# Kernel tuning notes

Hardware: AMD Instinct MI355X
Metric: run time of the kernel (lower is better)

The kernel has to match this reference:

```python
import jax, jax.numpy as jnp
import numpy as np

B, S, H, T, DI, HID, K, HEADS = 8, 1024, 768, 8, 64, 128, 8, 2
NEG = 1.0e12


def _build_adj(spans):
    # spans: [K,3] int; returns [K+1,K+1] edge multiplicity matrix (dst, src)
    s, e = spans[:, 0], spans[:, 1]
    same = (s[:, None] == s[None, :]) & (e[:, None] == e[None, :])
    # contain[i,j]: span i strictly contains span j (source appends this edge twice)
    contain = (s[:, None] <= s[None, :]) & (e[None, :] <= e[:, None]) & (~same)
    N = K + 1
    adj = jnp.eye(N, dtype=jnp.float32)                    # PyG add_self_loops
    adj = adj.at[1:, 0].add(1.0)                           # global -> span i
    adj = adj.at[0, 1:].add(1.0)                           # span i -> global
    adj = adj.at[1:, 1:].add(2.0 * contain.T.astype(jnp.float32))
    return adj


def _gat(x, adj, W, a_src, a_dst, b):
    # x [N,F]; adj [N,N] multiplicity with layout (dst, src). PyG GATConv math.
    N = x.shape[0]
    h = (x @ W).reshape(N, HEADS, -1)                      # [N,Hd,D]
    asrc = jnp.einsum('nhd,hd->nh', h, a_src)
    adst = jnp.einsum('nhd,hd->nh', h, a_dst)
    ee = jax.nn.leaky_relu(adst[:, None, :] + asrc[None, :, :], 0.2)  # [dst,src,Hd]
    logmult = jnp.where(adj > 0, jnp.log(jnp.maximum(adj, 1e-20)), 0.0)
    scores = jnp.where(adj[:, :, None] > 0, ee + logmult[:, :, None], -1e30)
    attn = jax.nn.softmax(scores, axis=1)                  # softmax over source nodes
    out = jnp.einsum('dsh,shf->dhf', attn, h).reshape(N, -1)
    return out + b


def _layernorm(x, g, bta):
    mu = x.mean(-1, keepdims=True)
    var = x.var(-1, keepdims=True)
    return (x - mu) / jnp.sqrt(var + 1e-5) * g + bta


def _forward(hidden, attention_mask, spans, W1, a_src1, a_dst1, b1, ln_g, ln_b,
             W2, a_src2, a_dst2, b2, dense_W, dense_b,
             g_centers, g_sigmas, g_weights, corr):
    start, end, etype = spans[..., 0], spans[..., 1], spans[..., 2]  # [B,K]
    pos = jnp.arange(S)
    span_mask = ((pos[None, None, :] >= start[..., None]) &
                 (pos[None, None, :] <= end[..., None])).astype(hidden.dtype)  # [B,K,S]
    span_len = (end - start + 1).astype(hidden.dtype)
    span_feat = jnp.einsum('bks,bsh->bkh', span_mask, hidden) / span_len[..., None]
    global_feat = hidden.mean(axis=1, keepdims=True)                 # [B,1,H]
    nodes = jnp.concatenate([global_feat, span_feat], axis=1)        # [B,K+1,H]
    adj = jax.vmap(_build_adj)(spans)                                # [B,K+1,K+1]

    g1 = jax.vmap(lambda x, a: _gat(x, a, W1, a_src1, a_dst1, b1))(nodes, adj)
    g1 = _layernorm(jax.nn.relu(g1), ln_g, ln_b)
    g2 = jax.vmap(lambda x, a: _gat(x, a, W2, a_src2, a_dst2, b2))(g1, adj)
    g2 = jax.nn.relu(g2)
    enhanced = g2.mean(axis=1)                                       # per-graph mean pool [B,2*HID]

    cover = span_mask.sum(axis=1)                                    # [B,S] how many spans cover token s
    token_enh = cover[..., None] * enhanced[:, None, :]              # [B,S,2*HID]
    combined = jnp.concatenate([hidden, token_enh], axis=-1)

    qk = (combined @ dense_W + dense_b).reshape(B, S, T, 2 * DI)
    qw, kw = qk[..., :DI], qk[..., DI:]

    # RoPE (sin/cos interleaved exactly as in source)
    inv = jnp.power(10000.0, -2.0 * jnp.arange(DI // 2) / DI)
    ang = pos[:, None].astype(jnp.float32) * inv[None, :]            # [S,DI/2]
    sin = jnp.repeat(jnp.sin(ang), 2, axis=-1)[None, :, None, :]     # [1,S,1,DI]
    cos = jnp.repeat(jnp.cos(ang), 2, axis=-1)[None, :, None, :]

    def rot(v):
        v2 = jnp.stack([-v[..., 1::2], v[..., ::2]], axis=-1).reshape(v.shape)
        return v * cos + v2 * sin

    qw, kw = rot(qw), rot(kw)

    logits = jnp.einsum('bmtd,bntd->btmn', qw, kw)                   # [B,T,S,S]

    # multi-modal gaussian kernel span maps (vectorized over batch/span/component)
    pf = pos.astype(jnp.float32)
    dxs = pf[None, None, None, :] - start[..., None, None] - g_centers[None, None, :, None]
    dxe = pf[None, None, None, :] - end[..., None, None] - g_centers[None, None, :, None]
    Ksr = g_weights[None, None, :, None] * jnp.exp(-0.5 * (dxs / g_sigmas[None, None, :, None]) ** 2)
    Ken = g_weights[None, None, :, None] * jnp.exp(-0.5 * (dxe / g_sigmas[None, None, :, None]) ** 2)
    gmap = jnp.einsum('bkcm,bkcn->bkmn', Ksr, Ken)                   # [B,K,S,S]
    corr_span = corr[etype]                                          # [B,K,T]
    logits = logits + jnp.einsum('bkt,bkmn->btmn', corr_span, gmap)

    pad = attention_mask[:, None, None, :]                           # key-dim-only mask (as in source)
    logits = logits * pad - (1.0 - pad) * NEG
    tril = jnp.tril(jnp.ones((S, S), logits.dtype), -1)
    logits = logits - tril * NEG
    return logits / jnp.sqrt(jnp.float32(DI))


def setup_inputs() -> dict:
    key = jax.random.key(0)
    ks = jax.random.split(key, 16)
    hidden = jax.random.normal(ks[0], (B, S, H), jnp.float32)
    attention_mask = jnp.ones((B, S), jnp.float32)
    start = jax.random.randint(ks[1], (B, K), 0, S - 32)
    length = jax.random.randint(ks[2], (B, K), 1, 16)
    spans = jnp.stack([start, start + length,
                       jax.random.randint(ks[3], (B, K), 0, T)], axis=-1).astype(jnp.int32)
    sd = 0.05
    return {
        'hidden': hidden,
        'attention_mask': attention_mask,
        'spans': spans,
        'W1': jax.random.normal(ks[4], (H, HEADS * HID), jnp.float32) * sd,
        'a_src1': jax.random.normal(ks[5], (HEADS, HID), jnp.float32) * sd,
        'a_dst1': jax.random.normal(ks[6], (HEADS, HID), jnp.float32) * sd,
        'b1': jnp.zeros((HEADS * HID,), jnp.float32),
        'ln_g': jnp.ones((HEADS * HID,), jnp.float32),
        'ln_b': jnp.zeros((HEADS * HID,), jnp.float32),
        'W2': jax.random.normal(ks[7], (HEADS * HID, HEADS * HID), jnp.float32) * sd,
        'a_src2': jax.random.normal(ks[8], (HEADS, HID), jnp.float32) * sd,
        'a_dst2': jax.random.normal(ks[9], (HEADS, HID), jnp.float32) * sd,
        'b2': jnp.zeros((HEADS * HID,), jnp.float32),
        'dense_W': jax.random.normal(ks[10], (H + HEADS * HID, T * 2 * DI), jnp.float32) * sd,
        'dense_b': jnp.zeros((T * 2 * DI,), jnp.float32),
        'g_centers': jnp.array([0.0, 0.0], jnp.float32),
        'g_sigmas': jnp.array([1.0, 3.0], jnp.float32),
        'g_weights': jnp.array([0.5, 0.5], jnp.float32),
        'corr': jnp.eye(T, dtype=jnp.float32),
    }


def reference(hidden, attention_mask, spans, W1, a_src1, a_dst1, b1, ln_g, ln_b,
              W2, a_src2, a_dst2, b2, dense_W, dense_b,
              g_centers, g_sigmas, g_weights, corr):
    return _forward(hidden, attention_mask, spans, W1, a_src1, a_dst1, b1, ln_g, ln_b,
                    W2, a_src2, a_dst2, b2, dense_W, dense_b,
                    g_centers, g_sigmas, g_weights, corr)
```

## Files before the change

kernel.cpp:

```cpp
#include <hip/hip_runtime.h>
#include <cstdint>
#include <cstddef>

#define BB 8
#define SS 1024
#define HH 768
#define TT 8
#define DII 64
#define HIDD 128
#define KSP 8
#define NHEADS 2
#define NNODES 9
#define GDIM 256
#define CDIM 1024
#define DAUGP 96
#define NEGV 1e12f

using bf16x8 = __attribute__((ext_vector_type(8))) __bf16;
using f32x4  = __attribute__((ext_vector_type(4))) float;

static __device__ inline unsigned short f2bf(float x) {
  union { float f; unsigned u; } v; v.f = x;
  unsigned r = v.u + 0x7fff + ((v.u >> 16) & 1);
  return (unsigned short)(r >> 16);
}

__global__ void kc1b_cvt_partial(const float* __restrict__ hidden,
                                 unsigned short* __restrict__ hbf,
                                 float* __restrict__ part) {
  int z = blockIdx.x, b = blockIdx.y, tid = threadIdx.x;
  const float* hb = hidden + (size_t)b * SS * HH;
  unsigned short* ho = hbf + (size_t)b * SS * HH;
  #pragma unroll
  for (int j = 0; j < 3; j++) {
    int c = tid + j * 256;
    float acc = 0.f;
    #pragma unroll 8
    for (int r = z * 64; r < z * 64 + 64; r++) {
      float v = hb[(size_t)r * HH + c];
      ho[(size_t)r * HH + c] = f2bf(v);
      acc += v;
    }
    part[((size_t)b * 16 + z) * HH + c] = acc;
  }
}

__global__ void kc2_cvt_wtop(const float* __restrict__ dense_W, unsigned short* __restrict__ WtopT) {
  __shared__ float t[32][33];
  int k0 = blockIdx.x * 32, n0 = blockIdx.y * 32;
  int tid = threadIdx.x;
  int r = tid >> 3, c4 = (tid & 7) * 4;
  float4 v = *(const float4*)&dense_W[(size_t)(k0 + r) * CDIM + n0 + c4];
  t[r][c4 + 0] = v.x; t[r][c4 + 1] = v.y; t[r][c4 + 2] = v.z; t[r][c4 + 3] = v.w;
  __syncthreads();
  int ro = tid >> 3, co4 = (tid & 7) * 4;
  ushort4 o;
  o.x = f2bf(t[co4 + 0][ro]); o.y = f2bf(t[co4 + 1][ro]);
  o.z = f2bf(t[co4 + 2][ro]); o.w = f2bf(t[co4 + 3][ro]);
  *(ushort4*)&WtopT[(size_t)(n0 + ro) * HH + k0 + co4] = o;
}

__global__ void k1a_spans(const float* __restrict__ hidden, const int* __restrict__ spans,
                          float* __restrict__ nodes, float* __restrict__ cover) {
  int k = blockIdx.x, b = blockIdx.y, tid = threadIdx.x;
  __shared__ int sp[KSP * 3];
  if (tid < KSP * 3) sp[tid] = spans[b * KSP * 3 + tid];
  __syncthreads();
  if (tid < 128) {
    int s = k * 128 + tid;
    float c = 0.f;
    #pragma unroll
    for (int kk = 0; kk < KSP; kk++)
      c += (s >= sp[kk * 3] && s <= sp[kk * 3 + 1]) ? 1.f : 0.f;
    cover[b * SS + s] = c;
  }
  int st = sp[k * 3], en = sp[k * 3 + 1];
  float inv = 1.f / (float)(en - st + 1);
  const float* hb = hidden + (size_t)b * SS * HH;
  #pragma unroll
  for (int ci = 0; ci < 3; ci++) {
    int c = tid + ci * 256;
    float a = 0.f;
    #pragma unroll
    for (int j = 0; j < 16; j++) {
      int s = st + j;
      int sc = (s <= en) ? s : en;
      float v = hb[(size_t)sc * HH + c];
      a += (s <= en) ? v : 0.f;
    }
    nodes[((size_t)b * NNODES + (k + 1)) * HH + c] = a * inv;
  }
}

__global__ __launch_bounds__(512) void k2_gat(
    const float* __restrict__ part, const float* __restrict__ nodes_g,
    const int* __restrict__ spans,
    const float* __restrict__ W1, const float* __restrict__ a_src1,
    const float* __restrict__ a_dst1, const float* __restrict__ b1,
    const float* __restrict__ ln_g, const float* __restrict__ ln_b,
    const float* __restrict__ W2, const float* __restrict__ a_src2,
    const float* __restrict__ a_dst2, const float* __restrict__ b2,
    float* __restrict__ enhg) {
  int b = blockIdx.x, tid = threadIdx.x;
  __shared__ __align__(16) float nod[NNODES * HH];
  __shared__ __align__(16) float hbuf[NNODES * GDIM];
  __shared__ __align__(16) float gbuf[NNODES * GDIM];
  __shared__ __align__(16) float pbuf[2 * NNODES * GDIM];
  __shared__ float asrc[NNODES * NHEADS], adst[NNODES * NHEADS];
  __shared__ float adjm[NNODES * NNODES];
  __shared__ float attn[NNODES * NNODES * NHEADS];
  __shared__ float mu_s[NNODES], rs_s[NNODES];
  __shared__ int sp[KSP * 3];
  if (tid < KSP * 3) sp[tid] = spans[b * KSP * 3 + tid];
  for (int c = tid; c < HH; c += 512) {
    float s = 0.f;
    #pragma unroll
    for (int z = 0; z < 16; z++) s += part[((size_t)b * 16 + z) * HH + c];
    nod[c] = s * (1.f / (float)SS);
  }
  for (int i = tid; i < (NNODES - 1) * HH; i += 512)
    nod[HH + i] = nodes_g[(size_t)b * NNODES * HH + HH + i];
  __syncthreads();
  {
    int col = tid & 255, h = tid >> 8;
    float acc[NNODES];
    #pragma unroll
    for (int n = 0; n < NNODES; n++) acc[n] = 0.f;
    int dlo = h * 384;
    #pragma unroll 2
    for (int d0 = dlo; d0 < dlo + 384; d0 += 4) {
      float4 nv[NNODES];
      #pragma unroll
      for (int n = 0; n < NNODES; n++) nv[n] = *(const float4*)&nod[n * HH + d0];
      float w0 = W1[(size_t)(d0 + 0) * GDIM + col];
      float w1 = W1[(size_t)(d0 + 1) * GDIM + col];
      float w2 = W1[(size_t)(d0 + 2) * GDIM + col];
      float w3 = W1[(size_t)(d0 + 3) * GDIM + col];
      #pragma unroll
      for (int n = 0; n < NNODES; n++)
        acc[n] += nv[n].x * w0 + nv[n].y * w1 + nv[n].z * w2 + nv[n].w * w3;
    }
    #pragma unroll
    for (int n = 0; n < NNODES; n++) pbuf[(h * NNODES + n) * GDIM + col] = acc[n];
  }
  __syncthreads();
  if (tid < GDIM) {
    #pragma unroll
    for (int n = 0; n < NNODES; n++)
      hbuf[n * GDIM + tid] = pbuf[n * GDIM + tid] + pbuf[(NNODES + n) * GDIM + tid];
  } else if (tid < 256 + NNODES * NNODES) {
    int q = tid - 256;
    int i = q / NNODES, j = q % NNODES;
    float a = (i == j) ? 1.f : 0.f;
    if (i > 0 && j == 0) a += 1.f;
    if (i == 0 && j > 0) a += 1.f;
    if (i > 0 && j > 0 && i != j) {
      int x = j - 1, y = i - 1;
      int sx = sp[x * 3], ex = sp[x * 3 + 1], sy = sp[y * 3], ey = sp[y * 3 + 1];
      bool same = (sx == sy) && (ex == ey);
      if (sx <= sy && ey <= ex && !same) a += 2.f;
    }
    adjm[q] = a;
  }
  __syncthreads();
  if (tid < NNODES * NHEADS) {
    int n = tid >> 1, hd = tid & 1;
    float sa = 0.f, sd = 0.f;
    #pragma unroll 8
    for (int f = 0; f < HIDD; f++) {
      float v = hbuf[n * GDIM + hd * HIDD + f];
      sa += v * a_src1[hd * HIDD + f];
      sd += v * a_dst1[hd * HIDD + f];
    }
    asrc[tid] = sa; adst[tid] = sd;
  }
  __syncthreads();
  if (tid < NNODES * NHEADS) {
    int d = tid >> 1, hd = tid & 1;
    float sc[NNODES]; float mx = -1e30f;
    for (int s2 = 0; s2 < NNODES; s2++) {
      float a = adjm[d * NNODES + s2]; float v;
      if (a > 0.f) {
        float e = adst[d * 2 + hd] + asrc[s2 * 2 + hd];
        e = (e > 0.f) ? e : 0.2f * e;
        v = e + __logf(a);
      } else v = -1e30f;
      sc[s2] = v; mx = fmaxf(mx, v);
    }
    float ssum = 0.f;
    for (int s2 = 0; s2 < NNODES; s2++) { float ex = __expf(sc[s2] - mx); sc[s2] = ex; ssum += ex; }
    float inv = 1.f / ssum;
    for (int s2 = 0; s2 < NNODES; s2++) attn[(d * NNODES + s2) * NHEADS + hd] = sc[s2] * inv;
  }
  __syncthreads();
  if (tid < 256) {
    int hd = tid >> 7;
    float bbv = b1[tid];
    for (int d = 0; d < NNODES; d++) {
      float acc = bbv;
      #pragma unroll
      for (int s2 = 0; s2 < NNODES; s2++)
        acc += attn[(d * NNODES + s2) * NHEADS + hd] * hbuf[s2 * GDIM + tid];
      gbuf[d * GDIM + tid] = fmaxf(acc, 0.f);
    }
  }
  __syncthreads();
  if (tid < NNODES) {
    float s1 = 0.f, s2v = 0.f;
    #pragma unroll 8
    for (int o = 0; o < GDIM; o++) { float v = gbuf[tid * GDIM + o]; s1 += v; s2v += v * v; }
    float mu = s1 / (float)GDIM;
    float var = s2v / (float)GDIM - mu * mu;
    mu_s[tid] = mu; rs_s[tid] = rsqrtf(var + 1e-5f);
  }
  __syncthreads();
  if (tid < 256) {
    float g = ln_g[tid], bt = ln_b[tid];
    for (int d = 0; d < NNODES; d++)
      gbuf[d * GDIM + tid] = (gbuf[d * GDIM + tid] - mu_s[d]) * rs_s[d] * g + bt;
  }
  __syncthreads();
  {
    int col = tid & 255, h = tid >> 8;
    float acc[NNODES];
    #pragma unroll
    for (int n = 0; n < NNODES; n++) acc[n] = 0.f;
    int dlo = h * 128;
    #pragma unroll 2
    for (int d0 = dlo; d0 < dlo + 128; d0 += 4) {
      float4 nv[NNODES];
      #pragma unroll
      for (int n = 0; n < NNODES; n++) nv[n] = *(const float4*)&gbuf[n * GDIM + d0];
      float w0 = W2[(size_t)(d0 + 0) * GDIM + col];
      float w1 = W2[(size_t)(d0 + 1) * GDIM + col];
      float w2 = W2[(size_t)(d0 + 2) * GDIM + col];
      float w3 = W2[(size_t)(d0 + 3) * GDIM + col];
      #pragma unroll
      for (int n = 0; n < NNODES; n++)
        acc[n] += nv[n].x * w0 + nv[n].y * w1 + nv[n].z * w2 + nv[n].w * w3;
    }
    #pragma unroll
    for (int n = 0; n < NNODES; n++) pbuf[(h * NNODES + n) * GDIM + col] = acc[n];
  }
  __syncthreads();
  if (tid < GDIM) {
    #pragma unroll
    for (int n = 0; n < NNODES; n++)
      hbuf[n * GDIM + tid] = pbuf[n * GDIM + tid] + pbuf[(NNODES + n) * GDIM + tid];
  }
  __syncthreads();
  if (tid < NNODES * NHEADS) {
    int n = tid >> 1, hd = tid & 1;
    float sa = 0.f, sd = 0.f;
    #pragma unroll 8
    for (int f = 0; f < HIDD; f++) {
      float v = hbuf[n * GDIM + hd * HIDD + f];
      sa += v * a_src2[hd * HIDD + f];
      sd += v * a_dst2[hd * HIDD + f];
    }
    asrc[tid] = sa; adst[tid] = sd;
  }
  __syncthreads();
  if (tid < NNODES * NHEADS) {
    int d = tid >> 1, hd = tid & 1;
    float sc[NNODES]; float mx = -1e30f;
    for (int s2 = 0; s2 < NNODES; s2++) {
      float a = adjm[d * NNODES + s2]; float v;
      if (a > 0.f) {
        float e = adst[d * 2 + hd] + asrc[s2 * 2 + hd];
        e = (e > 0.f) ? e : 0.2f * e;
        v = e + __logf(a);
      } else v = -1e30f;
      sc[s2] = v; mx = fmaxf(mx, v);
    }
    float ssum = 0.f;
    for (int s2 = 0; s2 < NNODES; s2++) { float ex = __expf(sc[s2] - mx); sc[s2] = ex; ssum += ex; }
    float inv = 1.f / ssum;
    for (int s2 = 0; s2 < NNODES; s2++) attn[(d * NNODES + s2) * NHEADS + hd] = sc[s2] * inv;
  }
  __syncthreads();
  if (tid < 256) {
    int hd = tid >> 7;
    float bbv = b2[tid];
    float msum = 0.f;
    for (int d = 0; d < NNODES; d++) {
      float acc = bbv;
      #pragma unroll
      for (int s2 = 0; s2 < NNODES; s2++)
        acc += attn[(d * NNODES + s2) * NHEADS + hd] * hbuf[s2 * GDIM + tid];
      msum += fmaxf(acc, 0.f);
    }
    enhg[b * GDIM + tid] = msum / 9.f;
  }
}

__global__ void k2b_e2(const float* __restrict__ enhg, const float* __restrict__ dense_W,
                       float* __restrict__ E2) {
  int b = blockIdx.y, tid = threadIdx.x;
  int o = blockIdx.x * 256 + tid;
  __shared__ __align__(16) float eh[GDIM];
  eh[tid] = enhg[b * GDIM + tid];
  __syncthreads();
  float acc = 0.f;
  #pragma unroll 2
  for (int d = 0; d < GDIM; d += 4) {
    float4 ev = *(const float4*)&eh[d];
    acc += ev.x * dense_W[(size_t)(HH + d + 0) * CDIM + o];
    acc += ev.y * dense_W[(size_t)(HH + d + 1) * CDIM + o];
    acc += ev.z * dense_W[(size_t)(HH + d + 2) * CDIM + o];
    acc += ev.w * dense_W[(size_t)(HH + d + 3) * CDIM + o];
  }
  E2[b * CDIM + o] = acc;
}

__global__ __launch_bounds__(256) void k3_dense(
    const unsigned short* __restrict__ hbf, const unsigned short* __restrict__ WtopT,
    const float* __restrict__ dense_b, const float* __restrict__ cover,
    const float* __restrict__ E2,
    unsigned short* __restrict__ Qa, unsigned short* __restrict__ Ka) {
  __shared__ unsigned short As[128 * 40];
  __shared__ unsigned short Bs[128 * 40];
  int tid = threadIdx.x;
  int n0 = blockIdx.x * 128, m0 = blockIdx.y * 128;
  int wave = tid >> 6, lane = tid & 63;
  int wr = wave >> 1, wc = wave & 1;
  int colL = lane & 15, quad = lane >> 4;
  f32x4 acc[4][4];
  #pragma unroll
  for (int i = 0; i < 4; i++)
    #pragma unroll
    for (int j = 0; j < 4; j++) { acc[i][j][0] = 0.f; acc[i][j][1] = 0.f; acc[i][j][2] = 0.f; acc[i][j][3] = 0.f; }
  for (int k0 = 0; k0 < HH; k0 += 32) {
    uint4 va[2], vb[2];
    #pragma unroll
    for (int it = 0; it < 2; it++) {
      int idx = tid + it * 256;
      int r = idx >> 2, seg = idx & 3;
      va[it] = *(const uint4*)(hbf + (size_t)(m0 + r) * HH + k0 + seg * 8);
      vb[it] = *(const uint4*)(WtopT + (size_t)(n0 + r) * HH + k0 + seg * 8);
    }
    __syncthreads();
    #pragma unroll
    for (int it = 0; it < 2; it++) {
      int idx = tid + it * 256;
      int r = idx >> 2, seg = idx & 3;
      *(uint4*)&As[r * 40 + seg * 8] = va[it];
      *(uint4*)&Bs[r * 40 + seg * 8] = vb[it];
    }
    __syncthreads();
    bf16x8 af[4], bf[4];
    #pragma unroll
    for (int tm = 0; tm < 4; tm++)
      af[tm] = *(const bf16x8*)&As[(wr * 64 + tm * 16 + colL) * 40 + quad * 8];
    #pragma unroll
    for (int tn = 0; tn < 4; tn++)
      bf[tn] = *(const bf16x8*)&Bs[(wc * 64 + tn * 16 + colL) * 40 + quad * 8];
    #pragma unroll
    for (int tm = 0; tm < 4; tm++)
      #pragma unroll
      for (int tn = 0; tn < 4; tn++)
        acc[tm][tn] = __builtin_amdgcn_mfma_f32_16x16x32_bf16(af[tm], bf[tn], acc[tm][tn], 0, 0, 0);
  }
  int b = m0 >> 10;
  const float LOG1E4_32 = 0.28782313662425576f;
  unsigned short* __restrict__ dst = (wc == 0) ? Qa : Ka;
  #pragma unroll
  for (int tn = 0; tn < 4; tn++) {
    int col = n0 + wc * 64 + tn * 16 + colL;
    float e2 = E2[b * CDIM + col];
    float db = dense_b[col];
    int t = col >> 7;
    int dd = tn * 16 + colL;
    int i0 = dd >> 1;
    float inv = __expf(-(float)i0 * LOG1E4_32);
    float sgn = (dd & 1) ? 1.f : -1.f;
    size_t tbase = (size_t)(b * TT + t) * SS;
    #pragma unroll
    for (int tm = 0; tm < 4; tm++) {
      int rbase = m0 + wr * 64 + tm * 16 + quad * 4;
      #pragma unroll
      for (int r = 0; r < 4; r++) {
        int m = rbase + r;
        int s = m & 1023;
        float w = acc[tm][tn][r] + cover[m] * e2 + db;
        float p = __shfl_xor(w, 1, 64);
        float sn, cs;
        __sincosf((float)s * inv, &sn, &cs);
        float o = w * cs + sgn * p * sn;
        dst[(tbase + s) * DAUGP + dd] = f2bf(o);
      }
    }
  }
}

__global__ void k4g_gauss(const int* __restrict__ spans, const float* __restrict__ corr,
                          const float* __restrict__ gc, const float* __restrict__ gs,
                          const float* __restrict__ gw,
                          unsigned short* __restrict__ Qa, unsigned short* __restrict__ Ka) {
  int tid = threadIdx.x;
  int g = tid >> 5, lane = tid & 31;
  int row = blockIdx.x * 8 + g;
  int b = row >> 10, s = row & 1023;
  int j = lane & 15;
  int kp = j >> 1, c = j & 1;
  int st = spans[(b * KSP + kp) * 3 + 0];
  int en = spans[(b * KSP + kp) * 3 + 1];
  int et = spans[(b * KSP + kp) * 3 + 2];
  float sig = gs[c], wgt = gw[c], ce = gc[c];
  if (lane < 16) {
    float dx = ((float)(s - st) - ce) / sig;
    float e = wgt * __expf(-0.5f * dx * dx);
    #pragma unroll
    for (int t = 0; t < TT; t++) {
      size_t base = ((size_t)(b * TT + t) * SS + s) * DAUGP;
      Qa[base + 64 + j] = f2bf(corr[et * TT + t] * e);
      Qa[base + 80 + j] = 0;
    }
  } else {
    float dx = ((float)(s - en) - ce) / sig;
    unsigned short bv = f2bf(wgt * __expf(-0.5f * dx * dx));
    #pragma unroll
    for (int t = 0; t < TT; t++) {
      size_t base = ((size_t)(b * TT + t) * SS + s) * DAUGP;
      Ka[base + 64 + j] = bv;
      Ka[base + 80 + j] = 0;
    }
  }
}

__global__ __launch_bounds__(256) void k5_logits(
    const unsigned short* __restrict__ Qa, const unsigned short* __restrict__ Ka,
    const float* __restrict__ amask, float* __restrict__ out) {
  int bz = blockIdx.z; int b = bz >> 3;
  int n0 = blockIdx.x * 128, m0 = blockIdx.y * 128;
  int tid = threadIdx.x;
  if (n0 + 127 < m0) {
    int r0 = tid >> 5, c4 = (tid & 31) * 4;
    float4 pv = *(const float4*)&amask[b * SS + n0 + c4];
    float4 o;
    o.x = (-(1.f - pv.x) * NEGV - NEGV) * 0.125f;
    o.y = (-(1.f - pv.y) * NEGV - NEGV) * 0.125f;
    o.z = (-(1.f - pv.z) * NEGV - NEGV) * 0.125f;
    o.w = (-(1.f - pv.w) * NEGV - NEGV) * 0.125f;
    for (int r = r0; r < 128; r += 8)
      *(float4*)&out[((size_t)bz * SS + m0 + r) * SS + n0 + c4] = o;
    return;
  }
  __shared__ unsigned short Qs[128 * 104];
  __shared__ unsigned short Ks[128 * 104];
  const unsigned short* Qrow = Qa + ((size_t)bz * SS + m0) * DAUGP;
  const unsigned short* Krow = Ka + ((size_t)bz * SS + n0) * DAUGP;
  #pragma unroll
  for (int it = 0; it < 6; it++) {
    int idx = tid + it * 256;
    int r = idx / 12, seg = idx % 12;
    uint4 vq = *(const uint4*)(Qrow + (size_t)r * DAUGP + seg * 8);
    uint4 vk = *(const uint4*)(Krow + (size_t)r * DAUGP + seg * 8);
    *(uint4*)&Qs[r * 104 + seg * 8] = vq;
    *(uint4*)&Ks[r * 104 + seg * 8] = vk;
  }
  __syncthreads();
  int wave = tid >> 6, lane = tid & 63;
  int wr = wave >> 1, wc = wave & 1;
  int colL = lane & 15, quad = lane >> 4;
  f32x4 acc[4][4];
  #pragma unroll
  for (int i = 0; i < 4; i++)
    #pragma unroll
    for (int j = 0; j < 4; j++) { acc[i][j][0] = 0.f; acc[i][j][1] = 0.f; acc[i][j][2] = 0.f; acc[i][j][3] = 0.f; }
  #pragma unroll
  for (int ks = 0; ks < 3; ks++) {
    bf16x8 af[4], bf[4];
    #pragma unroll
    for (int tm = 0; tm < 4; tm++)
      af[tm] = *(const bf16x8*)&Qs[(wr * 64 + tm * 16 + colL) * 104 + ks * 32 + quad * 8];
    #pragma unroll
    for (int tn = 0; tn < 4; tn++)
      bf[tn] = *(const bf16x8*)&Ks[(wc * 64 + tn * 16 + colL) * 104 + ks * 32 + quad * 8];
    #pragma unroll
    for (int tm = 0; tm < 4; tm++)
      #pragma unroll
      for (int tn = 0; tn < 4; tn++)
        acc[tm][tn] = __builtin_amdgcn_mfma_f32_16x16x32_bf16(af[tm], bf[tn], acc[tm][tn], 0, 0, 0);
  }
  #pragma unroll
  for (int tn = 0; tn < 4; tn++) {
    int col = n0 + wc * 64 + tn * 16 + colL;
    float p = amask[b * SS + col];
    float negp = -(1.f - p) * NEGV;
    #pragma unroll
    for (int tm = 0; tm < 4; tm++) {
      int rbase = m0 + wr * 64 + tm * 16 + quad * 4;
      #pragma unroll
      for (int r = 0; r < 4; r++) {
        int m = rbase + r;
        float v = acc[tm][tn][r] * p + negp;
        if (col < m) v -= NEGV;
        out[((size_t)bz * SS + m) * SS + col] = v * 0.125f;
      }
    }
  }
}

extern "C" void kernel_launch(void* const* d_in, const int* in_sizes, int n_in,
                              void* d_out, int out_size, void* d_ws, size_t ws_size,
                              hipStream_t stream) {
  const float* hidden  = (const float*)d_in[0];
  const float* amask   = (const float*)d_in[1];
  const int*   spans   = (const int*)d_in[2];
  const float* W1      = (const float*)d_in[3];
  const float* a_src1  = (const float*)d_in[4];
  const float* a_dst1  = (const float*)d_in[5];
  const float* b1      = (const float*)d_in[6];
  const float* ln_g    = (const float*)d_in[7];
  const float* ln_b    = (const float*)d_in[8];
  const float* W2      = (const float*)d_in[9];
  const float* a_src2  = (const float*)d_in[10];
  const float* a_dst2  = (const float*)d_in[11];
  const float* b2      = (const float*)d_in[12];
  const float* dense_W = (const float*)d_in[13];
  const float* dense_b = (const float*)d_in[14];
  const float* gc      = (const float*)d_in[15];
  const float* gs      = (const float*)d_in[16];
  const float* gw      = (const float*)d_in[17];
  const float* corr    = (const float*)d_in[18];

  char* wsb = (char*)d_ws;
  unsigned short* hbf  = (unsigned short*)wsb;                wsb += (size_t)BB * SS * HH * 2;
  unsigned short* WtopT= (unsigned short*)wsb;                wsb += (size_t)CDIM * HH * 2;
  unsigned short* Qa   = (unsigned short*)wsb;                wsb += (size_t)BB * TT * SS * DAUGP * 2;
  unsigned short* Ka   = (unsigned short*)wsb;                wsb += (size_t)BB * TT * SS * DAUGP * 2;
  float* nodes         = (float*)wsb;                         wsb += (size_t)BB * NNODES * HH * 4;
  float* cover         = (float*)wsb;                         wsb += (size_t)BB * SS * 4;
  float* E2            = (float*)wsb;                         wsb += (size_t)BB * CDIM * 4;
  float* enhg          = (float*)wsb;                         wsb += (size_t)BB * GDIM * 4;
  float* part          = (float*)wsb;                         wsb += (size_t)BB * 16 * HH * 4;
  float* outp = (float*)d_out;

  kc1b_cvt_partial<<<dim3(16, BB), 256, 0, stream>>>(hidden, hbf, part);
  kc2_cvt_wtop<<<dim3(HH / 32, CDIM / 32), 256, 0, stream>>>(dense_W, WtopT);
  k1a_spans<<<dim3(KSP, BB), 256, 0, stream>>>(hidden, spans, nodes, cover);
  k4g_gauss<<<(BB * SS) / 8, 256, 0, stream>>>(spans, corr, gc, gs, gw, Qa, Ka);
  k2_gat<<<BB, 512, 0, stream>>>(part, nodes, spans, W1, a_src1, a_dst1, b1, ln_g, ln_b,
                                 W2, a_src2, a_dst2, b2, enhg);
  k2b_e2<<<dim3(CDIM / 256, BB), 256, 0, stream>>>(enhg, dense_W, E2);
  k3_dense<<<dim3(CDIM / 128, (BB * SS) / 128), 256, 0, stream>>>(hbf, WtopT, dense_b,
                                                                  cover, E2, Qa, Ka);
  k5_logits<<<dim3(8, 8, BB * TT), 256, 0, stream>>>(Qa, Ka, amask, outp);
}
```

Before: 559.9 us.

## Merge prep kernels into one launch and fold E2 projection into GAT kernel

Four independent preprocessing kernels (bf16 conversion with partial sums, weight transpose, span pooling, gaussian feature fill) are merged into one kernel that dispatches on block index. The E2 projection is moved into the tail of the GAT kernel, so the enhg round trip and a separate launch go away. The GAT matmul loops also get a larger unroll. This cuts launch overhead and lets small workloads run side by side, but the E2 product now runs on only 8 blocks, which may serialize that step.

```diff
diff --git a/kernel.cpp b/kernel.cpp
--- a/kernel.cpp
+++ b/kernel.cpp
@@ -25,70 +25,110 @@
   return (unsigned short)(r >> 16);
 }
 
-__global__ void kc1b_cvt_partial(const float* __restrict__ hidden,
-                                 unsigned short* __restrict__ hbf,
-                                 float* __restrict__ part) {
-  int z = blockIdx.x, b = blockIdx.y, tid = threadIdx.x;
-  const float* hb = hidden + (size_t)b * SS * HH;
-  unsigned short* ho = hbf + (size_t)b * SS * HH;
-  #pragma unroll
-  for (int j = 0; j < 3; j++) {
-    int c = tid + j * 256;
-    float acc = 0.f;
-    #pragma unroll 8
-    for (int r = z * 64; r < z * 64 + 64; r++) {
-      float v = hb[(size_t)r * HH + c];
-      ho[(size_t)r * HH + c] = f2bf(v);
-      acc += v;
-    }
-    part[((size_t)b * 16 + z) * HH + c] = acc;
-  }
-}
-
-__global__ void kc2_cvt_wtop(const float* __restrict__ dense_W, unsigned short* __restrict__ WtopT) {
-  __shared__ float t[32][33];
-  int k0 = blockIdx.x * 32, n0 = blockIdx.y * 32;
-  int tid = threadIdx.x;
-  int r = tid >> 3, c4 = (tid & 7) * 4;
-  float4 v = *(const float4*)&dense_W[(size_t)(k0 + r) * CDIM + n0 + c4];
-  t[r][c4 + 0] = v.x; t[r][c4 + 1] = v.y; t[r][c4 + 2] = v.z; t[r][c4 + 3] = v.w;
-  __syncthreads();
-  int ro = tid >> 3, co4 = (tid & 7) * 4;
-  ushort4 o;
-  o.x = f2bf(t[co4 + 0][ro]); o.y = f2bf(t[co4 + 1][ro]);
-  o.z = f2bf(t[co4 + 2][ro]); o.w = f2bf(t[co4 + 3][ro]);
-  *(ushort4*)&WtopT[(size_t)(n0 + ro) * HH + k0 + co4] = o;
-}
-
-__global__ void k1a_spans(const float* __restrict__ hidden, const int* __restrict__ spans,
-                          float* __restrict__ nodes, float* __restrict__ cover) {
-  int k = blockIdx.x, b = blockIdx.y, tid = threadIdx.x;
-  __shared__ int sp[KSP * 3];
-  if (tid < KSP * 3) sp[tid] = spans[b * KSP * 3 + tid];
-  __syncthreads();
-  if (tid < 128) {
-    int s = k * 128 + tid;
-    float c = 0.f;
-    #pragma unroll
-    for (int kk = 0; kk < KSP; kk++)
-      c += (s >= sp[kk * 3] && s <= sp[kk * 3 + 1]) ? 1.f : 0.f;
-    cover[b * SS + s] = c;
-  }
-  int st = sp[k * 3], en = sp[k * 3 + 1];
-  float inv = 1.f / (float)(en - st + 1);
-  const float* hb = hidden + (size_t)b * SS * HH;
-  #pragma unroll
-  for (int ci = 0; ci < 3; ci++) {
-    int c = tid + ci * 256;
-    float a = 0.f;
-    #pragma unroll
-    for (int j = 0; j < 16; j++) {
-      int s = st + j;
-      int sc = (s <= en) ? s : en;
-      float v = hb[(size_t)sc * HH + c];
-      a += (s <= en) ? v : 0.f;
-    }
-    nodes[((size_t)b * NNODES + (k + 1)) * HH + c] = a * inv;
+__global__ __launch_bounds__(256) void kprep(
+    const float* __restrict__ hidden, const float* __restrict__ dense_W,
+    const int* __restrict__ spans, const float* __restrict__ corr,
+    const float* __restrict__ gc, const float* __restrict__ gs,
+    const float* __restrict__ gw,
+    unsigned short* __restrict__ hbf, unsigned short* __restrict__ WtopT,
+    float* __restrict__ part, float* __restrict__ nodes, float* __restrict__ cover,
+    unsigned short* __restrict__ Qa, unsigned short* __restrict__ Ka) {
+  int blk = blockIdx.x, tid = threadIdx.x;
+  if (blk < 128) {
+    int z = blk & 15, b = blk >> 4;
+    const float* hb = hidden + (size_t)b * SS * HH;
+    unsigned short* ho = hbf + (size_t)b * SS * HH;
+    #pragma unroll
+    for (int j = 0; j < 3; j++) {
+      int c = tid + j * 256;
+      float acc = 0.f;
+      #pragma unroll 8
+      for (int r = z * 64; r < z * 64 + 64; r++) {
+        float v = hb[(size_t)r * HH + c];
+        ho[(size_t)r * HH + c] = f2bf(v);
+        acc += v;
+      }
+      part[((size_t)b * 16 + z) * HH + c] = acc;
+    }
+  } else if (blk < 128 + 768) {
+    __shared__ float t[32][33];
+    int q = blk - 128;
+    int k0 = (q % 24) * 32, n0 = (q / 24) * 32;
+    int r = tid >> 3, c4 = (tid & 7) * 4;
+    float4 v = *(const float4*)&dense_W[(size_t)(k0 + r) * CDIM + n0 + c4];
+    t[r][c4 + 0] = v.x; t[r][c4 + 1] = v.y; t[r][c4 + 2] = v.z; t[r][c4 + 3] = v.w;
+    __syncthreads();
+    int ro = tid >> 3, co4 = (tid & 7) * 4;
+    ushort4 o;
+    o.x = f2bf(t[co4 + 0][ro]); o.y = f2bf(t[co4 + 1][ro]);
+    o.z = f2bf(t[co4 + 2][ro]); o.w = f2bf(t[co4 + 3][ro]);
+    *(ushort4*)&WtopT[(size_t)(n0 + ro) * HH + k0 + co4] = o;
+  } else {
+    int q = blk - 896;
+    int k = q & 7, b = q >> 3;
+    __shared__ int sp[KSP * 3];
+    if (tid < KSP * 3) sp[tid] = spans[b * KSP * 3 + tid];
+    __syncthreads();
+    if (tid < 128) {
+      int s = k * 128 + tid;
+      float c = 0.f;
+      #pragma unroll
+      for (int kk = 0; kk < KSP; kk++)
+        c += (s >= sp[kk * 3] && s <= sp[kk * 3 + 1]) ? 1.f : 0.f;
+      cover[b * SS + s] = c;
+    }
+    {
+      int st = sp[k * 3], en = sp[k * 3 + 1];
+      float inv = 1.f / (float)(en - st + 1);
+      const float* hb = hidden + (size_t)b * SS * HH;
+      #pragma unroll
+      for (int ci = 0; ci < 3; ci++) {
+        int c = tid + ci * 256;
+        float a = 0.f;
+        #pragma unroll
+        for (int j = 0; j < 16; j++) {
+          int s = st + j;
+          int sc = (s <= en) ? s : en;
+          float v = hb[(size_t)sc * HH + c];
+          a += (s <= en) ? v : 0.f;
+        }
+        nodes[((size_t)b * NNODES + (k + 1)) * HH + c] = a * inv;
+      }
+    }
+    {
+      int half = tid & 1, sl = tid >> 1;
+      int s = k * 128 + sl;
+      if (half == 0) {
+        #pragma unroll
+        for (int j = 0; j < 16; j++) {
+          int kp = j >> 1, c = j & 1;
+          int st = sp[kp * 3 + 0];
+          int et = sp[kp * 3 + 2];
+          float dx = ((float)(s - st) - gc[c]) / gs[c];
+          float e = gw[c] * __expf(-0.5f * dx * dx);
+          #pragma unroll
+          for (int t = 0; t < TT; t++) {
+            size_t base = ((size_t)(b * TT + t) * SS + s) * DAUGP;
+            Qa[base + 64 + j] = f2bf(corr[et * TT + t] * e);
+            Qa[base + 80 + j] = 0;
+          }
+        }
+      } else {
+        #pragma unroll
+        for (int j = 0; j < 16; j++) {
+          int kp = j >> 1, c = j & 1;
+          int en = sp[kp * 3 + 1];
+          float dx = ((float)(s - en) - gc[c]) / gs[c];
+          unsigned short bv = f2bf(gw[c] * __expf(-0.5f * dx * dx));
+          #pragma unroll
+          for (int t = 0; t < TT; t++) {
+            size_t base = ((size_t)(b * TT + t) * SS + s) * DAUGP;
+            Ka[base + 64 + j] = bv;
+            Ka[base + 80 + j] = 0;
+          }
+        }
+      }
+    }
   }
 }
 
@@ -100,12 +140,13 @@
     const float* __restrict__ ln_g, const float* __restrict__ ln_b,
     const float* __restrict__ W2, const float* __restrict__ a_src2,
     const float* __restrict__ a_dst2, const float* __restrict__ b2,
-    float* __restrict__ enhg) {
+    const float* __restrict__ dense_W, float* __restrict__ E2) {
   int b = blockIdx.x, tid = threadIdx.x;
   __shared__ __align__(16) float nod[NNODES * HH];
   __shared__ __align__(16) float hbuf[NNODES * GDIM];
   __shared__ __align__(16) float gbuf[NNODES * GDIM];
   __shared__ __align__(16) float pbuf[2 * NNODES * GDIM];
+  __shared__ __align__(16) float eh2[GDIM];
   __shared__ float asrc[NNODES * NHEADS], adst[NNODES * NHEADS];
   __shared__ float adjm[NNODES * NNODES];
   __shared__ float attn[NNODES * NNODES * NHEADS];
@@ -127,7 +168,7 @@
     #pragma unroll
     for (int n = 0; n < NNODES; n++) acc[n] = 0.f;
     int dlo = h * 384;
-    #pragma unroll 2
+    #pragma unroll 4
     for (int d0 = dlo; d0 < dlo + 384; d0 += 4) {
       float4 nv[NNODES];
       #pragma unroll
@@ -226,7 +267,7 @@
     #pragma unroll
     for (int n = 0; n < NNODES; n++) acc[n] = 0.f;
     int dlo = h * 128;
-    #pragma unroll 2
+    #pragma unroll 4
     for (int d0 = dlo; d0 < dlo + 128; d0 += 4) {
       float4 nv[NNODES];
       #pragma unroll
@@ -290,27 +331,24 @@
         acc += attn[(d * NNODES + s2) * NHEADS + hd] * hbuf[s2 * GDIM + tid];
       msum += fmaxf(acc, 0.f);
     }
-    enhg[b * GDIM + tid] = msum / 9.f;
-  }
-}
-
-__global__ void k2b_e2(const float* __restrict__ enhg, const float* __restrict__ dense_W,
-                       float* __restrict__ E2) {
-  int b = blockIdx.y, tid = threadIdx.x;
-  int o = blockIdx.x * 256 + tid;
-  __shared__ __align__(16) float eh[GDIM];
-  eh[tid] = enhg[b * GDIM + tid];
-  __syncthreads();
-  float acc = 0.f;
-  #pragma unroll 2
-  for (int d = 0; d < GDIM; d += 4) {
-    float4 ev = *(const float4*)&eh[d];
-    acc += ev.x * dense_W[(size_t)(HH + d + 0) * CDIM + o];
-    acc += ev.y * dense_W[(size_t)(HH + d + 1) * CDIM + o];
-    acc += ev.z * dense_W[(size_t)(HH + d + 2) * CDIM + o];
-    acc += ev.w * dense_W[(size_t)(HH + d + 3) * CDIM + o];
-  }
-  E2[b * CDIM + o] = acc;
+    eh2[tid] = msum / 9.f;
+  }
+  __syncthreads();
+  {
+    int o = tid;
+    float acc0 = 0.f, acc1 = 0.f;
+    #pragma unroll 4
+    for (int d = 0; d < GDIM; d += 4) {
+      float4 ev = *(const float4*)&eh2[d];
+      const float* w = &dense_W[(size_t)(HH + d) * CDIM + o];
+      acc0 += ev.x * w[0];          acc1 += ev.x * w[512];
+      acc0 += ev.y * w[CDIM];       acc1 += ev.y * w[CDIM + 512];
+      acc0 += ev.z * w[2 * CDIM];   acc1 += ev.z * w[2 * CDIM + 512];
+      acc0 += ev.w * w[3 * CDIM];   acc1 += ev.w * w[3 * CDIM + 512];
+    }
+    E2[b * CDIM + o] = acc0;
+    E2[b * CDIM + o + 512] = acc1;
+  }
 }
 
 __global__ __launch_bounds__(256) void k3_dense(
@@ -389,41 +427,6 @@
         float o = w * cs + sgn * p * sn;
         dst[(tbase + s) * DAUGP + dd] = f2bf(o);
       }
-    }
-  }
-}
-
-__global__ void k4g_gauss(const int* __restrict__ spans, const float* __restrict__ corr,
-                          const float* __restrict__ gc, const float* __restrict__ gs,
-                          const float* __restrict__ gw,
-                          unsigned short* __restrict__ Qa, unsigned short* __restrict__ Ka) {
-  int tid = threadIdx.x;
-  int g = tid >> 5, lane = tid & 31;
-  int row = blockIdx.x * 8 + g;
-  int b = row >> 10, s = row & 1023;
-  int j = lane & 15;
-  int kp = j >> 1, c = j & 1;
-  int st = spans[(b * KSP + kp) * 3 + 0];
-  int en = spans[(b * KSP + kp) * 3 + 1];
-  int et = spans[(b * KSP + kp) * 3 + 2];
-  float sig = gs[c], wgt = gw[c], ce = gc[c];
-  if (lane < 16) {
-    float dx = ((float)(s - st) - ce) / sig;
-    float e = wgt * __expf(-0.5f * dx * dx);
-    #pragma unroll
-    for (int t = 0; t < TT; t++) {
-      size_t base = ((size_t)(b * TT + t) * SS + s) * DAUGP;
-      Qa[base + 64 + j] = f2bf(corr[et * TT + t] * e);
-      Qa[base + 80 + j] = 0;
-    }
-  } else {
-    float dx = ((float)(s - en) - ce) / sig;
-    unsigned short bv = f2bf(wgt * __expf(-0.5f * dx * dx));
-    #pragma unroll
-    for (int t = 0; t < TT; t++) {
-      size_t base = ((size_t)(b * TT + t) * SS + s) * DAUGP;
-      Ka[base + 64 + j] = bv;
-      Ka[base + 80 + j] = 0;
     }
   }
 }
@@ -533,17 +536,13 @@
   float* nodes         = (float*)wsb;                         wsb += (size_t)BB * NNODES * HH * 4;
   float* cover         = (float*)wsb;                         wsb += (size_t)BB * SS * 4;
   float* E2            = (float*)wsb;                         wsb += (size_t)BB * CDIM * 4;
-  float* enhg          = (float*)wsb;                         wsb += (size_t)BB * GDIM * 4;
   float* part          = (float*)wsb;                         wsb += (size_t)BB * 16 * HH * 4;
   float* outp = (float*)d_out;
 
-  kc1b_cvt_partial<<<dim3(16, BB), 256, 0, stream>>>(hidden, hbf, part);
-  kc2_cvt_wtop<<<dim3(HH / 32, CDIM / 32), 256, 0, stream>>>(dense_W, WtopT);
-  k1a_spans<<<dim3(KSP, BB), 256, 0, stream>>>(hidden, spans, nodes, cover);
-  k4g_gauss<<<(BB * SS) / 8, 256, 0, stream>>>(spans, corr, gc, gs, gw, Qa, Ka);
+  kprep<<<960, 256, 0, stream>>>(hidden, dense_W, spans, corr, gc, gs, gw,
+                                 hbf, WtopT, part, nodes, cover, Qa, Ka);
   k2_gat<<<BB, 512, 0, stream>>>(part, nodes, spans, W1, a_src1, a_dst1, b1, ln_g, ln_b,
-                                 W2, a_src2, a_dst2, b2, enhg);
-  k2b_e2<<<dim3(CDIM / 256, BB), 256, 0, stream>>>(enhg, dense_W, E2);
+                                 W2, a_src2, a_dst2, b2, dense_W, E2);
   k3_dense<<<dim3(CDIM / 128, (BB * SS) / 128), 256, 0, stream>>>(hbf, WtopT, dense_b,
                                                                   cover, E2, Qa, Ka);
   k5_logits<<<dim3(8, 8, BB * TT), 256, 0, stream>>>(Qa, Ka, amask, outp);
```

After: 591.5 us. +5.6%, slower.
